# Kernel tuning notes

Measured on AMD Instinct MI355X. Metric: run time of the kernel, lower is better.

The kernel has to match this reference:

```python
import jax, jax.numpy as jnp
import numpy as np

B, L, C = 16, 2048, 1024
H, G, K = 16, 4, 5
GC = C // G          # group channels = 256
DH = C // H          # head channels = 64
PAD = K // 2         # 2


def conv1d(x, w, b, pad):
    # x: [N, Cin, L], w: [Cout, Cin, K]
    out = jax.lax.conv_general_dilated(x, w, (1,), [(pad, pad)],
                                       dimension_numbers=('NCH', 'OIH', 'NCH'))
    return out + b[None, :, None]


def setup_inputs() -> dict:
    key = jax.random.key(0)
    ks = jax.random.split(key, 16)
    s = 0.02
    inp = {
        'x': jax.random.normal(ks[0], (B, L, C), jnp.float32),
        'Wq': jax.random.normal(ks[1], (C, C), jnp.float32) * s,
        'bq': jnp.zeros((C,), jnp.float32),
        'Wk': jax.random.normal(ks[2], (C, C), jnp.float32) * s,
        'bk': jnp.zeros((C,), jnp.float32),
        'Wv': jax.random.normal(ks[3], (C, C), jnp.float32) * s,
        'bv': jnp.zeros((C,), jnp.float32),
        'Woff1': jax.random.normal(ks[4], (GC, GC, K), jnp.float32) * s,
        'boff1': jnp.zeros((GC,), jnp.float32),
        'Woff2': jax.random.normal(ks[5], (1, GC, 1), jnp.float32) * s,
        'boff2': jnp.zeros((1,), jnp.float32),
        'rpb_table': jax.random.normal(ks[6], (1, C, L), jnp.float32) * 0.02,
        'Wout': jax.random.normal(ks[7], (C, C), jnp.float32) * s,
        'bout': jnp.zeros((C,), jnp.float32),
    }
    return inp


def reference(x, Wq, bq, Wk, bk, Wv, bv, Woff1, boff1, Woff2, boff2,
              rpb_table, Wout, bout):
    xT = jnp.swapaxes(x, 1, 2)                        # [B, C, L]
    # conv1x1 q projection
    q = jnp.einsum('oc,bcl->bol', Wq, xT) + bq[None, :, None]
    gq = q.reshape(B * G, GC, L)                       # grouped queries
    # offset network: conv(k=5, pad=2) -> conv(k=1, pad=2) => length L+4
    h = conv1d(gq, Woff1, boff1, PAD)                  # [BG, GC, L]
    off = conv1d(h, Woff2, boff2, PAD)                 # [BG, 1, L+4]
    off = jnp.tanh(off[:, 0, :]) * K                   # offset_range_factor = kernel
    L4 = L + 2 * PAD
    grid = jnp.arange(L4, dtype=x.dtype)
    vgrid = grid[None, :] + off                        # [BG, L4]
    vs = 2.0 * vgrid / (L4 - 1) - 1.0                  # normalize with n = L+4 (as in source)
    # grid_sample bilinear, align_corners=False, zeros padding, over length L
    pos = ((vs + 1.0) * L - 1.0) / 2.0
    i0 = jnp.floor(pos)
    w1 = pos - i0
    i0 = i0.astype(jnp.int32)
    feats = xT.reshape(B * G, GC, L)

    def gather(idx):
        valid = ((idx >= 0) & (idx < L)).astype(x.dtype)
        idxc = jnp.clip(idx, 0, L - 1)
        g = jnp.take_along_axis(feats, jnp.broadcast_to(idxc[:, None, :], (B * G, GC, L4)), axis=2)
        return g * valid[:, None, :]

    samp = gather(i0) * (1.0 - w1)[:, None, :] + gather(i0 + 1) * w1[:, None, :]
    x_sampled = samp[:, :, :L].reshape(B, C, L)

    k = jnp.einsum('oc,bcl->bol', Wk, x_sampled) + bk[None, :, None]
    v = jnp.einsum('oc,bcl->bol', Wv, x_sampled) + bv[None, :, None] + rpb_table

    qh = q.reshape(B * H, DH, L)
    kh = k.reshape(B * H, DH, L)
    vh = v.reshape(B * H, DH, L)
    # attention over head-channel dims, contracting over sequence (faithful to source)
    scores = jnp.einsum('bil,bjl->bij', qh, kh) * (C ** -0.5)   # [BH, DH, DH]
    attn = jax.nn.softmax(scores, axis=-1)
    out = jnp.einsum('bij,bjl->bil', attn, vh)                  # [BH, DH, L]
    # rearrange '(b g) l c -> b c (g l)' with b=B, g=H, l=DH, c=L
    out = out.reshape(B, H, DH, L).transpose(0, 3, 1, 2).reshape(B, L, C)
    return out @ Wout.T + bout
```

## Files before the change

kernel.cpp:

```cpp
#include <hip/hip_runtime.h>
#include <hip/hip_bf16.h>
#include <stdint.h>

#define BATCH 16
#define SEQ   2048
#define CH    1024
#define NH    16
#define NG    4
#define KW    5
#define GCH   256
#define DHD   64
#define NBG   (BATCH*NG)
#define NBH   (BATCH*NH)
#define MROWS (BATCH*SEQ)

typedef __hip_bfloat16 bf16;
typedef float f32x4 __attribute__((ext_vector_type(4)));
typedef __bf16 bf16x8 __attribute__((ext_vector_type(8)));

__global__ __launch_bounds__(256)
void cvt_kernel(const float* __restrict__ in, bf16* __restrict__ out, int n)
{
    int i = (blockIdx.x*256 + threadIdx.x)*8;
    if (i >= n) return;
    float4 f0 = *(const float4*)(in+i);
    float4 f1 = *(const float4*)(in+i+4);
    union { bf16 b[8]; uint4 u; } pk;
    pk.b[0]=__float2bfloat16(f0.x); pk.b[1]=__float2bfloat16(f0.y);
    pk.b[2]=__float2bfloat16(f0.z); pk.b[3]=__float2bfloat16(f0.w);
    pk.b[4]=__float2bfloat16(f1.x); pk.b[5]=__float2bfloat16(f1.y);
    pk.b[6]=__float2bfloat16(f1.z); pk.b[7]=__float2bfloat16(f1.w);
    *(uint4*)(out+i) = pk.u;
}

__global__ void prep_weff_kernel(const float* __restrict__ W1, const float* __restrict__ b1,
                                 const float* __restrict__ w2, const float* __restrict__ b2,
                                 float* __restrict__ weff, float* __restrict__ wcst)
{
    int kk = blockIdx.x;
    int cj = threadIdx.x;
    float s = 0.f;
    for (int co=0; co<GCH; ++co)
        s += w2[co] * W1[((size_t)co*GCH + cj)*KW + kk];
    weff[kk*GCH + cj] = s;
    if (kk==0 && cj==0){
        float sb = 0.f;
        for (int co=0; co<GCH; ++co) sb += w2[co]*b1[co];
        wcst[0] = b2[0];
        wcst[1] = sb;
    }
}

template<int MODE>
__global__ __launch_bounds__(512, 2)
void gemm256_kernel(const bf16* __restrict__ A, const bf16* __restrict__ Wb,
                    const float* __restrict__ bias, const float* __restrict__ rpb,
                    void* __restrict__ outp)
{
    __shared__ __bf16 SM[3*16384];
    const int t = threadIdx.x;
    const int w = t>>6, l = t&63;
    const int wrow = w>>2, wcol = w&3;
    const int lr = l&15, kslot = l>>4;

    const int lin = blockIdx.x;
    const int xcd = lin&7, sblk = lin>>3;
    const int m0 = (xcd*16 + (sblk>>2))*256;
    const int n0 = (sblk&3)*256;

    const bf16* Ag = A  + (size_t)m0*CH;
    const bf16* Bg = Wb + (size_t)n0*CH;

    int srow[2], scol[2];
    #pragma unroll
    for (int r=0;r<2;++r){
        int o = (t + 512*r)*16;
        int e = o ^ (((o>>7)&3)<<4);
        srow[r] = e>>6;
        scol[r] = (e&63)>>1;
    }

    auto STAGE = [&](int tile, int buf){
        const int kt = tile*32;
        __bf16* ab = SM + buf*16384;
        __bf16* bb = ab + 8192;
        #pragma unroll
        for (int r=0;r<2;++r){
            __builtin_amdgcn_global_load_lds(
                (const __attribute__((address_space(1))) void*)(Ag + (size_t)srow[r]*CH + kt + scol[r]),
                (__attribute__((address_space(3))) void*)(ab + w*512 + r*4096), 16, 0, 0);
            __builtin_amdgcn_global_load_lds(
                (const __attribute__((address_space(1))) void*)(Bg + (size_t)srow[r]*CH + kt + scol[r]),
                (__attribute__((address_space(3))) void*)(bb + w*512 + r*4096), 16, 0, 0);
        }
    };

    f32x4 acc[8][4];
    #pragma unroll
    for (int i=0;i<8;++i)
        #pragma unroll
        for (int j=0;j<4;++j) acc[i][j] = (f32x4){0.f,0.f,0.f,0.f};

    STAGE(0, 0);
    STAGE(1, 1);
    asm volatile("s_waitcnt vmcnt(4)" ::: "memory");
    __builtin_amdgcn_s_barrier();
    __builtin_amdgcn_sched_barrier(0);

    const int NT = CH/32;
    for (int tt=0; tt<NT; ++tt){
        const int cur = tt%3;
        if (tt+2 < NT) STAGE(tt+2, (tt+2)%3);
        __builtin_amdgcn_sched_barrier(0);

        const __bf16* As_ = SM + cur*16384;
        const __bf16* Bs_ = As_ + 8192;
        bf16x8 af[8], bfr[4];
        #pragma unroll
        for (int fi=0; fi<8; ++fi){
            int row = wrow*128 + fi*16 + lr;
            int o = row*64 + kslot*16;
            o ^= ((o>>7)&3)<<4;
            af[fi] = *(const bf16x8*)(As_ + (o>>1));
        }
        #pragma unroll
        for (int fj=0; fj<4; ++fj){
            int row = wcol*64 + fj*16 + lr;
            int o = row*64 + kslot*16;
            o ^= ((o>>7)&3)<<4;
            bfr[fj] = *(const bf16x8*)(Bs_ + (o>>1));
        }
        asm volatile("s_waitcnt lgkmcnt(0)" ::: "memory");
        __builtin_amdgcn_sched_barrier(0);

        __builtin_amdgcn_s_setprio(1);
        #pragma unroll
        for (int fi=0; fi<8; ++fi)
            #pragma unroll
            for (int fj=0; fj<4; ++fj)
                acc[fi][fj] = __builtin_amdgcn_mfma_f32_16x16x32_bf16(af[fi], bfr[fj], acc[fi][fj], 0,0,0);
        __builtin_amdgcn_s_setprio(0);

        if (tt+2 < NT)      asm volatile("s_waitcnt vmcnt(4)" ::: "memory");
        else                asm volatile("s_waitcnt vmcnt(0)" ::: "memory");
        __builtin_amdgcn_s_barrier();
        __builtin_amdgcn_sched_barrier(0);
    }

    float bs[4];
    #pragma unroll
    for (int fj=0;fj<4;++fj) bs[fj] = bias[n0 + wcol*64 + fj*16 + lr];

    if constexpr (MODE == 2){
        const int bb2 = m0 >> 11;
        const int l0g = m0 & (SEQ-1);
        bf16* outT = (bf16*)outp;
        #pragma unroll
        for (int fi=0; fi<8; ++fi){
            int rowl = wrow*128 + fi*16 + kslot*4;
            #pragma unroll
            for (int fj=0; fj<4; ++fj){
                int col = n0 + wcol*64 + fj*16 + lr;
                union { bf16 h[4]; uint2 u; } pk;
                #pragma unroll
                for (int r=0;r<4;++r) pk.h[r] = __float2bfloat16(acc[fi][fj][r] + bs[fj]);
                *(uint2*)(outT + ((size_t)(bb2*CH + col))*SEQ + l0g + rowl) = pk.u;
            }
        }
    } else {
        #pragma unroll
        for (int fi=0; fi<8; ++fi){
            #pragma unroll
            for (int r=0;r<4;++r){
                int mg = m0 + wrow*128 + fi*16 + kslot*4 + r;
                int lseq = mg & (SEQ-1);
                #pragma unroll
                for (int fj=0; fj<4; ++fj){
                    int ng = n0 + wcol*64 + fj*16 + lr;
                    float v = acc[fi][fj][r] + bs[fj];
                    if constexpr (MODE==1) v += rpb[(size_t)ng*SEQ + lseq];
                    if constexpr (MODE==3)
                        ((float*)outp)[(size_t)mg*CH + ng] = v;
                    else
                        ((bf16*)outp)[(size_t)mg*CH + ng] = __float2bfloat16(v);
                }
            }
        }
    }
}

__global__ __launch_bounds__(256)
void offsets_kernel(const bf16* __restrict__ QT, const float* __restrict__ weff,
                    const float* __restrict__ wcst, float* __restrict__ posb)
{
    __shared__ float P5L[264][5];
    __shared__ float weffL[KW][GCH];
    const int t = threadIdx.x;
    const int chunk = blockIdx.x, bg = blockIdx.y;
    const int b = bg>>2, g = bg&3;
    const int l0 = chunk*256;

    for (int i = t; i < KW*GCH; i += 256) weffL[i/GCH][i&(GCH-1)] = weff[i];
    __syncthreads();

    const int j1 = l0 - 4 + t;
    const int j2 = l0 + 252 + t;
    const bool v1 = (j1 >= 0) & (j1 < SEQ);
    const bool v2 = (t < 4);
    float a1[KW] = {0,0,0,0,0};
    float a2[KW] = {0,0,0,0,0};
    const bf16* src = QT + ((size_t)(b*CH + g*GCH))*SEQ;
    for (int ch=0; ch<GCH; ++ch){
        const bf16* row = src + (size_t)ch*SEQ;
        float x1 = v1 ? __bfloat162float(row[j1 & (SEQ-1)]) : 0.f;
        #pragma unroll
        for (int kk=0;kk<KW;++kk) a1[kk] += x1*weffL[kk][ch];
        if (v2){
            float x2 = __bfloat162float(row[j2]);
            #pragma unroll
            for (int kk=0;kk<KW;++kk) a2[kk] += x2*weffL[kk][ch];
        }
    }
    #pragma unroll
    for (int kk=0;kk<KW;++kk) P5L[t][kk] = a1[kk];
    if (t < 4){
        #pragma unroll
        for (int kk=0;kk<KW;++kk) P5L[256+t][kk] = a2[kk];
    }
    __syncthreads();

    int lp = l0 + t;
    float b2 = wcst[0], wb1 = wcst[1];
    float o;
    if (lp < 2){
        o = b2;
    } else {
        float s = b2 + wb1;
        #pragma unroll
        for (int kk=0;kk<KW;++kk){
            int j = lp - 4 + kk;
            if (j >= 0 && j < SEQ) s += P5L[t+kk][kk];
        }
        o = s;
    }
    float off = tanhf(o) * (float)KW;
    posb[bg*SEQ + lp] = ((float)lp + off) * (2048.0f/2051.0f) - 0.5f;
}

__global__ __launch_bounds__(256)
void sample_kernel(const bf16* __restrict__ Xbf, const float* __restrict__ posb,
                   bf16* __restrict__ XS)
{
    const int ci = threadIdx.x, bg = blockIdx.y;
    const int b = bg>>2, g = bg&3;
    const int lp0 = blockIdx.x*8;
    #pragma unroll
    for (int s8=0; s8<8; ++s8){
        int lp = lp0 + s8;
        float p  = posb[bg*SEQ + lp];
        float fl = floorf(p);
        float w1 = p - fl;
        int i0 = (int)fl;
        float v = 0.f;
        if (i0 >= 0 && i0 < SEQ)
            v += __bfloat162float(Xbf[((size_t)(b*SEQ + i0))*CH + g*GCH + ci]) * (1.f - w1);
        if (i0+1 >= 0 && i0+1 < SEQ)
            v += __bfloat162float(Xbf[((size_t)(b*SEQ + i0 + 1))*CH + g*GCH + ci]) * w1;
        XS[((size_t)(b*SEQ + lp))*CH + g*GCH + ci] = __float2bfloat16(v);
    }
}

__global__ __launch_bounds__(256)
void attn_s_kernel(const bf16* __restrict__ QT, const bf16* __restrict__ KT,
                   bf16* __restrict__ Pbuf)
{
    __shared__ float Sc[64][69];
    __shared__ float red[64][4];
    __shared__ float mrow[64];
    __shared__ float sinv[64];
    const int t = threadIdx.x, w = t>>6, l = t&63;
    const int bh = blockIdx.x, b = bh>>4, h = bh&15;
    const bf16* q = QT + ((size_t)(b*CH + h*DHD))*SEQ;
    const bf16* k = KT + ((size_t)(b*CH + h*DHD))*SEQ;
    const int lr = l&15, lk = (l>>4)*8;

    f32x4 acc[4][4];
    #pragma unroll
    for (int i=0;i<4;++i)
        #pragma unroll
        for (int j=0;j<4;++j) acc[i][j] = (f32x4){0.f,0.f,0.f,0.f};

    for (int ks=0; ks<16; ++ks){
        int kp = w*512 + ks*32 + lk;
        bf16x8 af[4], bk8[4];
        #pragma unroll
        for (int i=0;i<4;++i) af[i]  = *(const bf16x8*)(q + (size_t)(i*16+lr)*SEQ + kp);
        #pragma unroll
        for (int j=0;j<4;++j) bk8[j] = *(const bf16x8*)(k + (size_t)(j*16+lr)*SEQ + kp);
        #pragma unroll
        for (int i=0;i<4;++i)
            #pragma unroll
            for (int j=0;j<4;++j)
                acc[i][j] = __builtin_amdgcn_mfma_f32_16x16x32_bf16(af[i], bk8[j], acc[i][j], 0,0,0);
    }
    for (int wv=0; wv<4; ++wv){
        if (w == wv){
            #pragma unroll
            for (int i=0;i<4;++i)
                #pragma unroll
                for (int j=0;j<4;++j)
                    #pragma unroll
                    for (int r=0;r<4;++r){
                        int m = i*16 + (l>>4)*4 + r, n = j*16 + lr;
                        if (wv==0) Sc[m][n]  = acc[i][j][r];
                        else       Sc[m][n] += acc[i][j][r];
                    }
        }
        __syncthreads();
    }
    const int r0 = t & 63, p = t >> 6;
    const float SCALE = 0.03125f;
    float mx = -1e30f;
    #pragma unroll
    for (int c=0;c<16;++c) mx = fmaxf(mx, Sc[r0][p*16+c]*SCALE);
    red[r0][p] = mx;
    __syncthreads();
    if (t < 64) mrow[t] = fmaxf(fmaxf(red[t][0],red[t][1]), fmaxf(red[t][2],red[t][3]));
    __syncthreads();
    float m = mrow[r0], s = 0.f;
    #pragma unroll
    for (int c=0;c<16;++c){
        float e = expf(Sc[r0][p*16+c]*SCALE - m);
        Sc[r0][p*16+c] = e;
        s += e;
    }
    red[r0][p] = s;
    __syncthreads();
    if (t < 64) sinv[t] = 1.f/(red[t][0]+red[t][1]+red[t][2]+red[t][3]);
    __syncthreads();
    float inv = sinv[r0];
    union { bf16 b[8]; uint4 u; } p0, p1;
    #pragma unroll
    for (int e=0;e<8;++e){
        p0.b[e] = __float2bfloat16(Sc[r0][p*16+e]*inv);
        p1.b[e] = __float2bfloat16(Sc[r0][p*16+8+e]*inv);
    }
    bf16* dst = Pbuf + (size_t)bh*4096 + r0*64 + p*16;
    *(uint4*)dst       = p0.u;
    *(uint4*)(dst + 8) = p1.u;
}

__global__ __launch_bounds__(256)
void attn_pv_kernel(const bf16* __restrict__ Pbuf, const bf16* __restrict__ V,
                    bf16* __restrict__ F)
{
    __shared__ __bf16 Pl[64][72];
    const int t = threadIdx.x, w = t>>6, l = t&63;
    const int chunk = blockIdx.x, bh = blockIdx.y;
    const int b = bh>>4, h = bh&15;
    {
        int row = t>>2, coff = (t&3)*16;
        const bf16* src = Pbuf + (size_t)bh*4096 + row*64 + coff;
        *(uint4*)&Pl[row][coff]   = *(const uint4*)src;
        *(uint4*)&Pl[row][coff+8] = *(const uint4*)(src+8);
    }
    __syncthreads();
    const int lr = l&15, lk = (l>>4)*8;
    const int lw = chunk*256 + w*64;

    f32x4 acc[4][4];
    #pragma unroll
    for (int i=0;i<4;++i)
        #pragma unroll
        for (int j=0;j<4;++j) acc[i][j] = (f32x4){0.f,0.f,0.f,0.f};

    #pragma unroll
    for (int ks=0; ks<2; ++ks){
        bf16x8 pf[4], vf[4];
        #pragma unroll
        for (int ni=0;ni<4;++ni) pf[ni] = *(const bf16x8*)&Pl[ni*16+lr][ks*32+lk];
        #pragma unroll
        for (int mi=0;mi<4;++mi)
            vf[mi] = *(const bf16x8*)(V + ((size_t)(b*SEQ + lw + mi*16 + lr))*CH + h*DHD + ks*32 + lk);
        #pragma unroll
        for (int mi=0;mi<4;++mi)
            #pragma unroll
            for (int ni=0;ni<4;++ni)
                acc[mi][ni] = __builtin_amdgcn_mfma_f32_16x16x32_bf16(vf[mi], pf[ni], acc[mi][ni], 0,0,0);
    }
    #pragma unroll
    for (int mi=0;mi<4;++mi){
        #pragma unroll
        for (int r=0;r<4;++r){
            int lpos = lw + mi*16 + (l>>4)*4 + r;
            #pragma unroll
            for (int ni=0;ni<4;++ni)
                F[((size_t)(b*SEQ + lpos))*CH + h*DHD + ni*16 + lr] =
                    __float2bfloat16(acc[mi][ni][r]);
        }
    }
}

extern "C" void kernel_launch(void* const* d_in, const int* in_sizes, int n_in,
                              void* d_out, int out_size, void* d_ws, size_t ws_size,
                              hipStream_t stream)
{
    const float* x   = (const float*)d_in[0];
    const float* Wq  = (const float*)d_in[1];
    const float* bq  = (const float*)d_in[2];
    const float* Wk  = (const float*)d_in[3];
    const float* bk  = (const float*)d_in[4];
    const float* Wv  = (const float*)d_in[5];
    const float* bv  = (const float*)d_in[6];
    const float* W1  = (const float*)d_in[7];
    const float* b1  = (const float*)d_in[8];
    const float* w2  = (const float*)d_in[9];
    const float* b2  = (const float*)d_in[10];
    const float* rpb = (const float*)d_in[11];
    const float* Wo  = (const float*)d_in[12];
    const float* bo  = (const float*)d_in[13];

    char* ws = (char*)d_ws;
    bf16*  Xbf  = (bf16*)(ws);
    bf16*  QT   = (bf16*)(ws + (size_t) 67108864);
    bf16*  XS   = (bf16*)(ws + (size_t)134217728);
    bf16*  VB   = (bf16*)(ws + (size_t)201326592);
    bf16*  Pbuf = (bf16*)(ws + (size_t)268435456);
    bf16*  wslot= (bf16*)(ws + (size_t)270532608);
    float* posb = (float*)(ws + (size_t)272629760);
    float* weff = (float*)(ws + (size_t)273154048);
    float* wcst = (float*)(ws + (size_t)273159168);
    bf16*  KT = Xbf;
    bf16*  Fb = XS;

    prep_weff_kernel<<<dim3(KW), dim3(GCH), 0, stream>>>(W1, b1, w2, b2, weff, wcst);
    cvt_kernel<<<dim3(MROWS*CH/8/256), 256, 0, stream>>>(x, Xbf, MROWS*CH);

    cvt_kernel<<<dim3(CH*CH/8/256), 256, 0, stream>>>(Wq, wslot, CH*CH);
    gemm256_kernel<2><<<dim3(512), 512, 0, stream>>>(Xbf, wslot, bq, nullptr, QT);

    offsets_kernel<<<dim3(SEQ/256, NBG), 256, 0, stream>>>(QT, weff, wcst, posb);
    sample_kernel<<<dim3(SEQ/8, NBG), 256, 0, stream>>>(Xbf, posb, XS);

    cvt_kernel<<<dim3(CH*CH/8/256), 256, 0, stream>>>(Wk, wslot, CH*CH);
    gemm256_kernel<2><<<dim3(512), 512, 0, stream>>>(XS, wslot, bk, nullptr, KT);

    cvt_kernel<<<dim3(CH*CH/8/256), 256, 0, stream>>>(Wv, wslot, CH*CH);
    gemm256_kernel<1><<<dim3(512), 512, 0, stream>>>(XS, wslot, bv, rpb, VB);

    attn_s_kernel<<<dim3(NBH), 256, 0, stream>>>(QT, KT, Pbuf);
    attn_pv_kernel<<<dim3(8, NBH), 256, 0, stream>>>(Pbuf, VB, Fb);

    cvt_kernel<<<dim3(CH*CH/8/256), 256, 0, stream>>>(Wo, wslot, CH*CH);
    gemm256_kernel<3><<<dim3(512), 512, 0, stream>>>(Fb, wslot, bo, nullptr, (float*)d_out);
}
```

Measured before the change: 725.7 us.

## Use BK=64 double-buffered GEMM tiles and vectorize offset conv reduction

The GEMM goes from a triple-buffered K=32 pipeline to double-buffered K=64 tiles with a new 8-way XOR swizzle. This halves the number of barrier and waitcnt iterations per tile, but the prefetch distance drops to one tile and the loop waits for vmcnt(0) every iteration. The offsets kernel is restructured so each thread loads 8 contiguous bf16 sequence positions per channel row with a vector load and accumulates over a 32-channel slice. Partial sums are reduced across 8 channel groups in shared memory, replacing scalar strided loads with coalesced vector loads.

```diff
diff --git a/kernel.cpp b/kernel.cpp
--- a/kernel.cpp
+++ b/kernel.cpp
@@ -18,6 +18,14 @@
 typedef float f32x4 __attribute__((ext_vector_type(4)));
 typedef __bf16 bf16x8 __attribute__((ext_vector_type(8)));
 
+__device__ __forceinline__ void unpack8(uint4 r, float* f){
+    uint32_t w0=r.x,w1=r.y,w2=r.z,w3=r.w;
+    f[0]=__uint_as_float(w0<<16); f[1]=__uint_as_float(w0&0xffff0000u);
+    f[2]=__uint_as_float(w1<<16); f[3]=__uint_as_float(w1&0xffff0000u);
+    f[4]=__uint_as_float(w2<<16); f[5]=__uint_as_float(w2&0xffff0000u);
+    f[6]=__uint_as_float(w3<<16); f[7]=__uint_as_float(w3&0xffff0000u);
+}
+
 __global__ __launch_bounds__(256)
 void cvt_kernel(const float* __restrict__ in, bf16* __restrict__ out, int n)
 {
@@ -57,11 +65,11 @@
                     const float* __restrict__ bias, const float* __restrict__ rpb,
                     void* __restrict__ outp)
 {
-    __shared__ __bf16 SM[3*16384];
+    __shared__ __bf16 SM[2*32768];
     const int t = threadIdx.x;
     const int w = t>>6, l = t&63;
     const int wrow = w>>2, wcol = w&3;
-    const int lr = l&15, kslot = l>>4;
+    const int lr = l&15, kq = l>>4;
 
     const int lin = blockIdx.x;
     const int xcd = lin&7, sblk = lin>>3;
@@ -71,21 +79,21 @@
     const bf16* Ag = A  + (size_t)m0*CH;
     const bf16* Bg = Wb + (size_t)n0*CH;
 
-    int srow[2], scol[2];
-    #pragma unroll
-    for (int r=0;r<2;++r){
+    int srow[4], scol[4];
+    #pragma unroll
+    for (int r=0;r<4;++r){
         int o = (t + 512*r)*16;
-        int e = o ^ (((o>>7)&3)<<4);
-        srow[r] = e>>6;
-        scol[r] = (e&63)>>1;
+        int e = o ^ (((o>>7)&7)<<4);
+        srow[r] = e>>7;
+        scol[r] = (e&127)>>1;
     }
 
     auto STAGE = [&](int tile, int buf){
-        const int kt = tile*32;
-        __bf16* ab = SM + buf*16384;
-        __bf16* bb = ab + 8192;
-        #pragma unroll
-        for (int r=0;r<2;++r){
+        const int kt = tile*64;
+        __bf16* ab = SM + buf*32768;
+        __bf16* bb = ab + 16384;
+        #pragma unroll
+        for (int r=0;r<4;++r){
             __builtin_amdgcn_global_load_lds(
                 (const __attribute__((address_space(1))) void*)(Ag + (size_t)srow[r]*CH + kt + scol[r]),
                 (__attribute__((address_space(3))) void*)(ab + w*512 + r*4096), 16, 0, 0);
@@ -102,47 +110,46 @@
         for (int j=0;j<4;++j) acc[i][j] = (f32x4){0.f,0.f,0.f,0.f};
 
     STAGE(0, 0);
-    STAGE(1, 1);
-    asm volatile("s_waitcnt vmcnt(4)" ::: "memory");
+    asm volatile("s_waitcnt vmcnt(0)" ::: "memory");
     __builtin_amdgcn_s_barrier();
     __builtin_amdgcn_sched_barrier(0);
 
-    const int NT = CH/32;
+    const int NT = CH/64;
     for (int tt=0; tt<NT; ++tt){
-        const int cur = tt%3;
-        if (tt+2 < NT) STAGE(tt+2, (tt+2)%3);
+        const int cur = tt&1;
+        if (tt+1 < NT) STAGE(tt+1, cur^1);
         __builtin_amdgcn_sched_barrier(0);
 
-        const __bf16* As_ = SM + cur*16384;
-        const __bf16* Bs_ = As_ + 8192;
-        bf16x8 af[8], bfr[4];
-        #pragma unroll
-        for (int fi=0; fi<8; ++fi){
-            int row = wrow*128 + fi*16 + lr;
-            int o = row*64 + kslot*16;
-            o ^= ((o>>7)&3)<<4;
-            af[fi] = *(const bf16x8*)(As_ + (o>>1));
-        }
-        #pragma unroll
-        for (int fj=0; fj<4; ++fj){
-            int row = wcol*64 + fj*16 + lr;
-            int o = row*64 + kslot*16;
-            o ^= ((o>>7)&3)<<4;
-            bfr[fj] = *(const bf16x8*)(Bs_ + (o>>1));
-        }
-        asm volatile("s_waitcnt lgkmcnt(0)" ::: "memory");
-        __builtin_amdgcn_sched_barrier(0);
-
-        __builtin_amdgcn_s_setprio(1);
-        #pragma unroll
-        for (int fi=0; fi<8; ++fi)
-            #pragma unroll
-            for (int fj=0; fj<4; ++fj)
-                acc[fi][fj] = __builtin_amdgcn_mfma_f32_16x16x32_bf16(af[fi], bfr[fj], acc[fi][fj], 0,0,0);
-        __builtin_amdgcn_s_setprio(0);
-
-        if (tt+2 < NT)      asm volatile("s_waitcnt vmcnt(4)" ::: "memory");
-        else                asm volatile("s_waitcnt vmcnt(0)" ::: "memory");
+        const __bf16* As_ = SM + cur*32768;
+        const __bf16* Bs_ = As_ + 16384;
+        #pragma unroll
+        for (int ks=0; ks<2; ++ks){
+            bf16x8 af[8], bfr[4];
+            #pragma unroll
+            for (int fi=0; fi<8; ++fi){
+                int row = wrow*128 + fi*16 + lr;
+                int byte = row*128 + ks*64 + kq*16;
+                byte ^= (row&7)<<4;
+                af[fi] = *(const bf16x8*)(As_ + (byte>>1));
+            }
+            #pragma unroll
+            for (int fj=0; fj<4; ++fj){
+                int row = wcol*64 + fj*16 + lr;
+                int byte = row*128 + ks*64 + kq*16;
+                byte ^= (row&7)<<4;
+                bfr[fj] = *(const bf16x8*)(Bs_ + (byte>>1));
+            }
+            asm volatile("s_waitcnt lgkmcnt(0)" ::: "memory");
+            __builtin_amdgcn_sched_barrier(0);
+            __builtin_amdgcn_s_setprio(1);
+            #pragma unroll
+            for (int fi=0; fi<8; ++fi)
+                #pragma unroll
+                for (int fj=0; fj<4; ++fj)
+                    acc[fi][fj] = __builtin_amdgcn_mfma_f32_16x16x32_bf16(af[fi], bfr[fj], acc[fi][fj], 0,0,0);
+            __builtin_amdgcn_s_setprio(0);
+        }
+        asm volatile("s_waitcnt vmcnt(0)" ::: "memory");
         __builtin_amdgcn_s_barrier();
         __builtin_amdgcn_sched_barrier(0);
     }
@@ -157,7 +164,7 @@
         bf16* outT = (bf16*)outp;
         #pragma unroll
         for (int fi=0; fi<8; ++fi){
-            int rowl = wrow*128 + fi*16 + kslot*4;
+            int rowl = wrow*128 + fi*16 + kq*4;
             #pragma unroll
             for (int fj=0; fj<4; ++fj){
                 int col = n0 + wcol*64 + fj*16 + lr;
@@ -172,7 +179,7 @@
         for (int fi=0; fi<8; ++fi){
             #pragma unroll
             for (int r=0;r<4;++r){
-                int mg = m0 + wrow*128 + fi*16 + kslot*4 + r;
+                int mg = m0 + wrow*128 + fi*16 + kq*4 + r;
                 int lseq = mg & (SEQ-1);
                 #pragma unroll
                 for (int fj=0; fj<4; ++fj){
@@ -193,44 +200,69 @@
 void offsets_kernel(const bf16* __restrict__ QT, const float* __restrict__ weff,
                     const float* __restrict__ wcst, float* __restrict__ posb)
 {
-    __shared__ float P5L[264][5];
+    __shared__ float P5R[8][272][5];
     __shared__ float weffL[KW][GCH];
     const int t = threadIdx.x;
     const int chunk = blockIdx.x, bg = blockIdx.y;
     const int b = bg>>2, g = bg&3;
     const int l0 = chunk*256;
 
-    for (int i = t; i < KW*GCH; i += 256) weffL[i/GCH][i&(GCH-1)] = weff[i];
-    __syncthreads();
-
-    const int j1 = l0 - 4 + t;
-    const int j2 = l0 + 252 + t;
-    const bool v1 = (j1 >= 0) & (j1 < SEQ);
-    const bool v2 = (t < 4);
-    float a1[KW] = {0,0,0,0,0};
-    float a2[KW] = {0,0,0,0,0};
-    const bf16* src = QT + ((size_t)(b*CH + g*GCH))*SEQ;
-    for (int ch=0; ch<GCH; ++ch){
-        const bf16* row = src + (size_t)ch*SEQ;
-        float x1 = v1 ? __bfloat162float(row[j1 & (SEQ-1)]) : 0.f;
-        #pragma unroll
-        for (int kk=0;kk<KW;++kk) a1[kk] += x1*weffL[kk][ch];
-        if (v2){
-            float x2 = __bfloat162float(row[j2]);
-            #pragma unroll
-            for (int kk=0;kk<KW;++kk) a2[kk] += x2*weffL[kk][ch];
-        }
-    }
-    #pragma unroll
-    for (int kk=0;kk<KW;++kk) P5L[t][kk] = a1[kk];
-    if (t < 4){
-        #pragma unroll
-        for (int kk=0;kk<KW;++kk) P5L[256+t][kk] = a2[kk];
-    }
-    __syncthreads();
-
-    int lp = l0 + t;
-    float b2 = wcst[0], wb1 = wcst[1];
+    for (int i = t; i < KW*GCH; i += 256) weffL[i>>8][i&255] = weff[i];
+    __syncthreads();
+
+    const int jg = t & 31, cg = t >> 5;
+
+    auto doblock = [&](int jb, int cgx){
+        const int j0 = l0 - 8 + jb*8;
+        float acc[8][KW];
+        #pragma unroll
+        for (int e=0;e<8;++e)
+            #pragma unroll
+            for (int kk=0;kk<KW;++kk) acc[e][kk] = 0.f;
+        const bf16* base = QT + ((size_t)(b*CH + g*GCH + cgx*32))*SEQ;
+        const bool safe = (j0 >= 0) && (j0 + 8 <= SEQ);
+        if (safe){
+            #pragma unroll 4
+            for (int i=0;i<32;++i){
+                float xv[8];
+                { union { bf16x8 v; uint4 u; } cv;
+                  cv.v = *(const bf16x8*)(base + (size_t)i*SEQ + j0);
+                  unpack8(cv.u, xv); }
+                float wk[KW];
+                #pragma unroll
+                for (int kk=0;kk<KW;++kk) wk[kk] = weffL[kk][cgx*32 + i];
+                #pragma unroll
+                for (int e=0;e<8;++e)
+                    #pragma unroll
+                    for (int kk=0;kk<KW;++kk) acc[e][kk] += xv[e]*wk[kk];
+            }
+        } else {
+            for (int i=0;i<32;++i){
+                float wk[KW];
+                #pragma unroll
+                for (int kk=0;kk<KW;++kk) wk[kk] = weffL[kk][cgx*32 + i];
+                #pragma unroll
+                for (int e=0;e<8;++e){
+                    int j = j0 + e;
+                    float xv = (j >= 0 && j < SEQ)
+                             ? __bfloat162float(base[(size_t)i*SEQ + j]) : 0.f;
+                    #pragma unroll
+                    for (int kk=0;kk<KW;++kk) acc[e][kk] += xv*wk[kk];
+                }
+            }
+        }
+        #pragma unroll
+        for (int e=0;e<8;++e)
+            #pragma unroll
+            for (int kk=0;kk<KW;++kk) P5R[cgx][jb*8+e][kk] = acc[e][kk];
+    };
+
+    doblock(jg, cg);
+    if (t < 16) doblock(32 + (t&1), t>>1);
+    __syncthreads();
+
+    const int lp = l0 + t;
+    const float b2 = wcst[0], wb1 = wcst[1];
     float o;
     if (lp < 2){
         o = b2;
@@ -239,7 +271,13 @@
         #pragma unroll
         for (int kk=0;kk<KW;++kk){
             int j = lp - 4 + kk;
-            if (j >= 0 && j < SEQ) s += P5L[t+kk][kk];
+            if (j >= 0 && j < SEQ){
+                int jp = t + 4 + kk;
+                float v = 0.f;
+                #pragma unroll
+                for (int c8=0;c8<8;++c8) v += P5R[c8][jp][kk];
+                s += v;
+            }
         }
         o = s;
     }
```

After: 602.6 us. -17.0%, faster.
